# Kernel optimization log

Measured on AMD Instinct MI355X. Metric: run time of the kernel, lower is better.

## Reference

```python
import jax, jax.numpy as jnp
import numpy as np

B, C, H, W = 8, 256, 64, 64
C8 = C // 8


def setup_inputs() -> dict:
    key = jax.random.key(0)
    ks = jax.random.split(key, 8)
    x = jax.random.normal(ks[0], (B, C, H, W), dtype=jnp.float32)
    # 1x1 convs == channel matmuls; store as [out_ch, in_ch] plus bias
    Wq = jax.random.normal(ks[1], (C8, C), dtype=jnp.float32) * (1.0 / np.sqrt(C))
    bq = jnp.zeros((C8,), dtype=jnp.float32)
    Wk = jax.random.normal(ks[2], (C8, C), dtype=jnp.float32) * (1.0 / np.sqrt(C))
    bk = jnp.zeros((C8,), dtype=jnp.float32)
    Wv = jax.random.normal(ks[3], (C, C), dtype=jnp.float32) * (1.0 / np.sqrt(C))
    bv = jnp.zeros((C,), dtype=jnp.float32)
    # gamma initialized to zero in the module, but use a nonzero value so the
    # attention branch actually contributes to the output being checked
    gamma = jnp.full((1,), 0.5, dtype=jnp.float32)
    return {"x": x, "Wq": Wq, "bq": bq, "Wk": Wk, "bk": bk, "Wv": Wv, "bv": bv, "gamma": gamma}


def reference(x, Wq, bq, Wk, bk, Wv, bv, gamma):
    b, c, h, w = x.shape
    n = h * w
    xf = x.reshape(b, c, n)                                  # [B, C, N]
    q = jnp.einsum('oc,bcn->bon', Wq, xf) + bq[None, :, None]  # [B, C8, N]
    k = jnp.einsum('oc,bcn->bon', Wk, xf) + bk[None, :, None]  # [B, C8, N]
    v = jnp.einsum('oc,bcn->bon', Wv, xf) + bv[None, :, None]  # [B, C,  N]
    # attention[b, i, j] = sum_d q[b, d, i] * k[b, d, j]  (no 1/sqrt(d) scaling!)
    scores = jnp.einsum('bdi,bdj->bij', q, k)                # [B, N, N]
    attn = jax.nn.softmax(scores, axis=-1)                   # softmax over j
    # out[b, c, i] = sum_j v[b, c, j] * attn[b, i, j]
    out = jnp.einsum('bcj,bij->bci', v, attn)                # [B, C, N]
    out = out.reshape(b, c, h, w)
    return gamma[0] * out + x
```

## Files before the change

### kernel.cpp

```cpp
#include <hip/hip_runtime.h>
#include <math.h>

#define BB 8
#define CC 256
#define NN 4096

typedef float f4 __attribute__((ext_vector_type(4)));
typedef short bh8 __attribute__((ext_vector_type(8)));

__device__ __forceinline__ unsigned short f2bf(float f) {
    unsigned u = __builtin_bit_cast(unsigned, f);
    u += 0x7fff + ((u >> 16) & 1);
    return (unsigned short)(u >> 16);
}
__device__ __forceinline__ unsigned packbf(float a, float b) {
    return (unsigned)f2bf(a) | ((unsigned)f2bf(b) << 16);
}

__device__ __forceinline__ float exp2_fast(float x) {
    float r;
    asm("v_exp_f32 %0, %1" : "=v"(r) : "v"(x));
    return r;
}

__global__ void prep_w_kernel(const float* __restrict__ Wq, const float* __restrict__ bq,
                              const float* __restrict__ Wk, const float* __restrict__ bk,
                              const float* __restrict__ Wv, const float* __restrict__ bv,
                              float* __restrict__ WcatT, float* __restrict__ bcat) {
    const float L2E = 1.4426950408889634f;
    int idx = blockIdx.x * 256 + threadIdx.x;
    if (idx < 320) {
        bcat[idx] = (idx < 32) ? bq[idx] * L2E : (idx < 64 ? bk[idx - 32] : bv[idx - 64]);
    }
    if (idx < 320 * 256) {
        int o = idx >> 8;
        int c = idx & 255;
        float v = (o < 32) ? Wq[o * 256 + c] * L2E
                           : (o < 64 ? Wk[(o - 32) * 256 + c] : Wv[(o - 64) * 256 + c]);
        WcatT[c * 320 + o] = v;
    }
}

__global__ __launch_bounds__(256, 2) void qkv_kernel(
    const float* __restrict__ x, const float* __restrict__ WcatT,
    const float* __restrict__ bcat,
    unsigned short* __restrict__ q64, unsigned short* __restrict__ k64,
    unsigned short* __restrict__ vC) {
    __shared__ float xs[256 * 64];
    __shared__ unsigned short qkl[64 * 128];
    unsigned short* vsl = (unsigned short*)xs;

    int blk = blockIdx.x;
    int b = blk >> 6;
    int i0 = (blk & 63) << 6;
    int t = threadIdx.x;

    const float* xb = x + ((size_t)b << 20);
    for (int idx = t; idx < 256 * 64; idx += 256) {
        int c = idx >> 6, ii = idx & 63;
        xs[idx] = xb[((size_t)c << 12) + i0 + ii];
    }
    __syncthreads();

    int to = t & 63;
    int tp = t >> 6;

    float acc[80];
#pragma unroll
    for (int uo = 0; uo < 5; ++uo) {
        float bias = bcat[to + 64 * uo];
#pragma unroll
        for (int pi = 0; pi < 16; ++pi) acc[uo * 16 + pi] = bias;
    }

    for (int c = 0; c < 256; ++c) {
        const float* wc = WcatT + c * 320 + to;
        float w0 = wc[0];
        float w1 = wc[64];
        float w2 = wc[128];
        float w3 = wc[192];
        float w4 = wc[256];
        const float4* xr = (const float4*)(xs + c * 64 + 16 * tp);
#pragma unroll
        for (int q = 0; q < 4; ++q) {
            float4 xv = xr[q];
#pragma unroll
            for (int e = 0; e < 4; ++e) {
                int pi = 4 * q + e;
                float xe = (e == 0) ? xv.x : (e == 1) ? xv.y : (e == 2) ? xv.z : xv.w;
                acc[0 * 16 + pi] += w0 * xe;
                acc[1 * 16 + pi] += w1 * xe;
                acc[2 * 16 + pi] += w2 * xe;
                acc[3 * 16 + pi] += w3 * xe;
                acc[4 * 16 + pi] += w4 * xe;
            }
        }
    }
    __syncthreads();

#pragma unroll
    for (int pi = 0; pi < 16; ++pi) {
        int ii = 16 * tp + pi;
        float v = acc[pi];
        unsigned short hi = f2bf(v);
        float vhi = __builtin_bit_cast(float, ((unsigned)hi) << 16);
        unsigned short lo = f2bf(v - vhi);
        if (to < 32) {
            qkl[ii * 128 + to] = hi;
            qkl[ii * 128 + 32 + to] = lo;
        } else {
            qkl[ii * 128 + 32 + to] = hi;
            qkl[ii * 128 + 64 + to] = lo;
        }
    }
#pragma unroll
    for (int uo = 1; uo < 5; ++uo) {
#pragma unroll
        for (int pi = 0; pi < 16; ++pi) {
            int c = to + 64 * (uo - 1);
            int ii = 16 * tp + pi;
            vsl[c * 66 + ii] = f2bf(acc[uo * 16 + pi]);
        }
    }
    __syncthreads();

    const unsigned* qk32 = (const unsigned*)qkl;
    unsigned* qb = (unsigned*)(q64 + ((size_t)(b * NN + i0)) * 64);
    unsigned* kb = (unsigned*)(k64 + ((size_t)(b * NN + i0)) * 64);
    for (int idx = t; idx < 64 * 32; idx += 256) {
        int row = idx >> 5, dw = idx & 31;
        qb[row * 32 + dw] = qk32[row * 64 + dw];
        kb[row * 32 + dw] = qk32[row * 64 + 32 + dw];
    }
    for (int idx = t; idx < 256 * 32; idx += 256) {
        int c = idx >> 5, dw = idx & 31;
        unsigned val = *(const unsigned*)(vsl + c * 66 + 2 * dw);
        int i = 2 * dw;
        int p = 32 * (i >> 5) + 8 * ((i >> 2) & 3) + 4 * ((i >> 4) & 1) + (i & 3);
        *(unsigned*)(vC + ((size_t)(b * CC + c)) * NN + i0 + p) = val;
    }
}

__global__ __launch_bounds__(256, 2) void attn_kernel(
    const unsigned short* __restrict__ q64, const unsigned short* __restrict__ k64,
    const unsigned short* __restrict__ vC, const float* __restrict__ x,
    const float* __restrict__ gamma, float* __restrict__ out) {
    __shared__ unsigned short vs[2][256 * 64];

    int t = threadIdx.x;
    int lane = t & 63;
    int w = t >> 6;
    int g = lane >> 4;
    int li = lane & 15;
    int blk = blockIdx.x;
    int b = blk & 7;
    int i0 = (blk >> 3) << 6;
    int qb = i0 + 16 * w;

    const unsigned short* vb = vC + ((size_t)b * CC) * NN;
    const unsigned short* kb = k64 + ((size_t)b * NN) * 64;

    bh8 qf[2];
#pragma unroll
    for (int s = 0; s < 2; ++s)
        qf[s] = *(const bh8*)(q64 + ((size_t)(b * NN + qb + li)) * 64 + s * 32 + 8 * g);

    const unsigned short* vsrcb[8];
#pragma unroll
    for (int s = 0; s < 8; ++s) {
        int c = 64 * w + 8 * s + (lane >> 3);
        int slot = (lane & 7) ^ (c & 7);
        vsrcb[s] = vb + (size_t)c * NN + slot * 8;
    }
    const unsigned short* ksrcb[8];
#pragma unroll
    for (int jt = 0; jt < 4; ++jt)
#pragma unroll
        for (int s = 0; s < 2; ++s)
            ksrcb[jt * 2 + s] = kb + (size_t)(16 * jt + li) * 64 + s * 32 + 8 * g;

    f4 acc[16];
#pragma unroll
    for (int ct = 0; ct < 16; ++ct) acc[ct] = (f4){0.f, 0.f, 0.f, 0.f};
    float m = -INFINITY, l = 0.f;

    auto stageV = [&](int buf, int j0) {
#pragma unroll
        for (int s = 0; s < 8; ++s) {
            __builtin_amdgcn_global_load_lds(
                (const __attribute__((address_space(1))) unsigned int*)(vsrcb[s] + j0),
                (__attribute__((address_space(3))) unsigned int*)(&vs[buf][(64 * w + 8 * s) * 64]),
                16, 0, 0);
        }
    };
    auto loadK = [&](bh8 (&kf)[4][2], int j0) {
        size_t joff = (size_t)j0 * 64;
#pragma unroll
        for (int jt = 0; jt < 4; ++jt)
#pragma unroll
            for (int s = 0; s < 2; ++s)
                kf[jt][s] = *(const bh8*)(ksrcb[jt * 2 + s] + joff);
    };
    auto qkComp = [&](f4 (&sOut)[4], bh8 (&kc)[4][2]) {
#pragma unroll
        for (int jt = 0; jt < 4; ++jt) {
            f4 a = {0.f, 0.f, 0.f, 0.f};
            a = __builtin_amdgcn_mfma_f32_16x16x32_bf16(kc[jt][0], qf[0], a, 0, 0, 0);
            a = __builtin_amdgcn_mfma_f32_16x16x32_bf16(kc[jt][1], qf[0], a, 0, 0, 0);
            a = __builtin_amdgcn_mfma_f32_16x16x32_bf16(kc[jt][0], qf[1], a, 0, 0, 0);
            sOut[jt] = a;
        }
    };

    bh8 kf0[4][2], kf1[4][2];
    f4 sA[4], sB[4];

    stageV(0, 0);
    loadK(kf0, 0);
    loadK(kf1, 64);
    qkComp(sA, kf0);
    __syncthreads();

    auto step = [&](int tt, bh8 (&kNext)[4][2], bh8 (&kLoad)[4][2],
                    f4 (&sCur)[4], f4 (&sNxt)[4], int buf) {
        if (tt < 63) stageV(buf ^ 1, (tt + 1) << 6);
        if (tt < 62) loadK(kLoad, (tt + 2) << 6);

        if (tt < 63) qkComp(sNxt, kNext);

        float mx = sCur[0][0];
#pragma unroll
        for (int jt = 0; jt < 4; ++jt)
#pragma unroll
            for (int e = 0; e < 4; ++e) mx = fmaxf(mx, sCur[jt][e]);
        if (!__all(mx <= m + 11.541561f)) {
            mx = fmaxf(mx, __shfl_xor(mx, 16));
            mx = fmaxf(mx, __shfl_xor(mx, 32));
            float mnew = fmaxf(m, mx);
            float sc = exp2_fast(m - mnew);
            l *= sc;
#pragma unroll
            for (int ct = 0; ct < 16; ++ct)
#pragma unroll
                for (int e = 0; e < 4; ++e) acc[ct][e] *= sc;
            m = mnew;
        }
        float sum = 0.f;
#pragma unroll
        for (int jt = 0; jt < 4; ++jt)
#pragma unroll
            for (int e = 0; e < 4; ++e) {
                float p = exp2_fast(sCur[jt][e] - m);
                sCur[jt][e] = p;
                sum += p;
            }
        l += sum;

        const char* vsb = (const char*)vs[buf];
#pragma unroll
        for (int h = 0; h < 2; ++h) {
            union { unsigned u[4]; bh8 v; } pf;
            pf.u[0] = packbf(sCur[2 * h + 0][0], sCur[2 * h + 0][1]);
            pf.u[1] = packbf(sCur[2 * h + 0][2], sCur[2 * h + 0][3]);
            pf.u[2] = packbf(sCur[2 * h + 1][0], sCur[2 * h + 1][1]);
            pf.u[3] = packbf(sCur[2 * h + 1][2], sCur[2 * h + 1][3]);
            bh8 pb = pf.v;
            __builtin_amdgcn_s_setprio(1);
#pragma unroll
            for (int ct = 0; ct < 16; ++ct) {
                int c = 16 * ct + li;
                int off = c * 128 + ((64 * h + 16 * g) ^ ((c & 7) << 4));
                bh8 vf = *(const bh8*)(vsb + off);
                acc[ct] = __builtin_amdgcn_mfma_f32_16x16x32_bf16(vf, pb, acc[ct], 0, 0, 0);
            }
            __builtin_amdgcn_s_setprio(0);
        }
        __syncthreads();
    };

    for (int tt = 0; tt < 64; tt += 2) {
        step(tt, kf1, kf0, sA, sB, 0);
        step(tt + 1, kf0, kf1, sB, sA, 1);
    }

    l += __shfl_xor(l, 16);
    l += __shfl_xor(l, 32);

    float gm = gamma[0];
    float rl = 1.f / l;
    const float* xb = x + ((size_t)b * CC) * NN;
    float* ob = out + ((size_t)b * CC) * NN;
    int i = qb + li;
#pragma unroll
    for (int ct = 0; ct < 16; ++ct)
#pragma unroll
        for (int e = 0; e < 4; ++e) {
            int c = 16 * ct + 4 * g + e;
            size_t idx = (size_t)c * NN + i;
            ob[idx] = gm * (acc[ct][e] * rl) + xb[idx];
        }
}

extern "C" void kernel_launch(void* const* d_in, const int* in_sizes, int n_in,
                              void* d_out, int out_size, void* d_ws, size_t ws_size,
                              hipStream_t stream) {
    const float* x = (const float*)d_in[0];
    const float* Wq = (const float*)d_in[1];
    const float* bq = (const float*)d_in[2];
    const float* Wk = (const float*)d_in[3];
    const float* bk = (const float*)d_in[4];
    const float* Wv = (const float*)d_in[5];
    const float* bv = (const float*)d_in[6];
    const float* gamma = (const float*)d_in[7];
    float* out = (float*)d_out;

    unsigned short* ws16 = (unsigned short*)d_ws;
    unsigned short* q64w = ws16;
    unsigned short* k64w = ws16 + 2097152;
    unsigned short* vCw = ws16 + 4194304;
    float* WcatT = (float*)((char*)d_ws + 25165824);
    float* bcat = WcatT + 81920;

    prep_w_kernel<<<320, 256, 0, stream>>>(Wq, bq, Wk, bk, Wv, bv, WcatT, bcat);
    qkv_kernel<<<BB * (NN / 64), 256, 0, stream>>>(x, WcatT, bcat, q64w, k64w, vCw);
    attn_kernel<<<512, 256, 0, stream>>>(q64w, k64w, vCw, x, gamma, out);
}
```

Baseline: 235.9 us.

## Load V fragments directly from global memory instead of staging through LDS

Removes the double-buffered LDS staging of V tiles and the per-step __syncthreads, having each wave load its V MFMA operands straight from global memory into registers in interleaved batches. The launch bound is lowered to one block per SM to make room for the extra V registers. The aim is to drop barrier and LDS traffic, at the cost that the four waves in a block now each read the full V tile from global/L2, giving redundant loads and exposed latency, plus lower occupancy.

```diff
diff --git a/kernel.cpp b/kernel.cpp
--- a/kernel.cpp
+++ b/kernel.cpp
@@ -141,12 +141,10 @@
     }
 }
 
-__global__ __launch_bounds__(256, 2) void attn_kernel(
+__global__ __launch_bounds__(256, 1) void attn_kernel(
     const unsigned short* __restrict__ q64, const unsigned short* __restrict__ k64,
     const unsigned short* __restrict__ vC, const float* __restrict__ x,
     const float* __restrict__ gamma, float* __restrict__ out) {
-    __shared__ unsigned short vs[2][256 * 64];
-
     int t = threadIdx.x;
     int lane = t & 63;
     int w = t >> 6;
@@ -165,41 +163,24 @@
     for (int s = 0; s < 2; ++s)
         qf[s] = *(const bh8*)(q64 + ((size_t)(b * NN + qb + li)) * 64 + s * 32 + 8 * g);
 
-    const unsigned short* vsrcb[8];
-#pragma unroll
-    for (int s = 0; s < 8; ++s) {
-        int c = 64 * w + 8 * s + (lane >> 3);
-        int slot = (lane & 7) ^ (c & 7);
-        vsrcb[s] = vb + (size_t)c * NN + slot * 8;
-    }
-    const unsigned short* ksrcb[8];
-#pragma unroll
-    for (int jt = 0; jt < 4; ++jt)
-#pragma unroll
-        for (int s = 0; s < 2; ++s)
-            ksrcb[jt * 2 + s] = kb + (size_t)(16 * jt + li) * 64 + s * 32 + 8 * g;
+    const unsigned short* kbase = kb + (size_t)li * 64 + 8 * g;
+    const unsigned short* vbase = vb + (size_t)li * NN + 8 * g;
 
     f4 acc[16];
 #pragma unroll
     for (int ct = 0; ct < 16; ++ct) acc[ct] = (f4){0.f, 0.f, 0.f, 0.f};
     float m = -INFINITY, l = 0.f;
 
-    auto stageV = [&](int buf, int j0) {
-#pragma unroll
-        for (int s = 0; s < 8; ++s) {
-            __builtin_amdgcn_global_load_lds(
-                (const __attribute__((address_space(1))) unsigned int*)(vsrcb[s] + j0),
-                (__attribute__((address_space(3))) unsigned int*)(&vs[buf][(64 * w + 8 * s) * 64]),
-                16, 0, 0);
-        }
-    };
     auto loadK = [&](bh8 (&kf)[4][2], int j0) {
         size_t joff = (size_t)j0 * 64;
 #pragma unroll
         for (int jt = 0; jt < 4; ++jt)
 #pragma unroll
             for (int s = 0; s < 2; ++s)
-                kf[jt][s] = *(const bh8*)(ksrcb[jt * 2 + s] + joff);
+                kf[jt][s] = *(const bh8*)(kbase + joff + jt * (16 * 64) + s * 32);
+    };
+    auto vload = [&](int ct, int h, int j0) -> bh8 {
+        return *(const bh8*)(vbase + (size_t)ct * (16 * NN) + j0 + 32 * h);
     };
     auto qkComp = [&](f4 (&sOut)[4], bh8 (&kc)[4][2]) {
 #pragma unroll
@@ -215,18 +196,20 @@
     bh8 kf0[4][2], kf1[4][2];
     f4 sA[4], sB[4];
 
-    stageV(0, 0);
     loadK(kf0, 0);
     loadK(kf1, 64);
     qkComp(sA, kf0);
-    __syncthreads();
 
     auto step = [&](int tt, bh8 (&kNext)[4][2], bh8 (&kLoad)[4][2],
-                    f4 (&sCur)[4], f4 (&sNxt)[4], int buf) {
-        if (tt < 63) stageV(buf ^ 1, (tt + 1) << 6);
+                    f4 (&sCur)[4], f4 (&sNxt)[4]) {
+        int j0 = tt << 6;
         if (tt < 62) loadK(kLoad, (tt + 2) << 6);
 
         if (tt < 63) qkComp(sNxt, kNext);
+
+        bh8 va[8], vb2[8];
+#pragma unroll
+        for (int ct = 0; ct < 8; ++ct) va[ct] = vload(ct, 0, j0);
 
         float mx = sCur[0][0];
 #pragma unroll
@@ -256,31 +239,46 @@
             }
         l += sum;
 
-        const char* vsb = (const char*)vs[buf];
-#pragma unroll
-        for (int h = 0; h < 2; ++h) {
-            union { unsigned u[4]; bh8 v; } pf;
-            pf.u[0] = packbf(sCur[2 * h + 0][0], sCur[2 * h + 0][1]);
-            pf.u[1] = packbf(sCur[2 * h + 0][2], sCur[2 * h + 0][3]);
-            pf.u[2] = packbf(sCur[2 * h + 1][0], sCur[2 * h + 1][1]);
-            pf.u[3] = packbf(sCur[2 * h + 1][2], sCur[2 * h + 1][3]);
-            bh8 pb = pf.v;
-            __builtin_amdgcn_s_setprio(1);
-#pragma unroll
-            for (int ct = 0; ct < 16; ++ct) {
-                int c = 16 * ct + li;
-                int off = c * 128 + ((64 * h + 16 * g) ^ ((c & 7) << 4));
-                bh8 vf = *(const bh8*)(vsb + off);
-                acc[ct] = __builtin_amdgcn_mfma_f32_16x16x32_bf16(vf, pb, acc[ct], 0, 0, 0);
-            }
-            __builtin_amdgcn_s_setprio(0);
-        }
-        __syncthreads();
+        union { unsigned u[4]; bh8 v; } pf0, pf1;
+        pf0.u[0] = packbf(sCur[0][0], sCur[0][1]);
+        pf0.u[1] = packbf(sCur[0][2], sCur[0][3]);
+        pf0.u[2] = packbf(sCur[1][0], sCur[1][1]);
+        pf0.u[3] = packbf(sCur[1][2], sCur[1][3]);
+        pf1.u[0] = packbf(sCur[2][0], sCur[2][1]);
+        pf1.u[1] = packbf(sCur[2][2], sCur[2][3]);
+        pf1.u[2] = packbf(sCur[3][0], sCur[3][1]);
+        pf1.u[3] = packbf(sCur[3][2], sCur[3][3]);
+        bh8 pb0 = pf0.v, pb1 = pf1.v;
+
+#pragma unroll
+        for (int ct = 0; ct < 8; ++ct) vb2[ct] = vload(ct + 8, 0, j0);
+        __builtin_amdgcn_s_setprio(1);
+#pragma unroll
+        for (int ct = 0; ct < 8; ++ct)
+            acc[ct] = __builtin_amdgcn_mfma_f32_16x16x32_bf16(va[ct], pb0, acc[ct], 0, 0, 0);
+        __builtin_amdgcn_s_setprio(0);
+#pragma unroll
+        for (int ct = 0; ct < 8; ++ct) va[ct] = vload(ct, 1, j0);
+        __builtin_amdgcn_s_setprio(1);
+#pragma unroll
+        for (int ct = 0; ct < 8; ++ct)
+            acc[ct + 8] = __builtin_amdgcn_mfma_f32_16x16x32_bf16(vb2[ct], pb0, acc[ct + 8], 0, 0, 0);
+        __builtin_amdgcn_s_setprio(0);
+#pragma unroll
+        for (int ct = 0; ct < 8; ++ct) vb2[ct] = vload(ct + 8, 1, j0);
+        __builtin_amdgcn_s_setprio(1);
+#pragma unroll
+        for (int ct = 0; ct < 8; ++ct)
+            acc[ct] = __builtin_amdgcn_mfma_f32_16x16x32_bf16(va[ct], pb1, acc[ct], 0, 0, 0);
+#pragma unroll
+        for (int ct = 0; ct < 8; ++ct)
+            acc[ct + 8] = __builtin_amdgcn_mfma_f32_16x16x32_bf16(vb2[ct], pb1, acc[ct + 8], 0, 0, 0);
+        __builtin_amdgcn_s_setprio(0);
     };
 
     for (int tt = 0; tt < 64; tt += 2) {
-        step(tt, kf1, kf0, sA, sB, 0);
-        step(tt + 1, kf0, kf1, sB, sA, 1);
+        step(tt, kf1, kf0, sA, sB);
+        step(tt + 1, kf0, kf1, sB, sA);
     }
 
     l += __shfl_xor(l, 16);
```

Result: slower. 661.6 us (+180.5%).

## Compute QKV projection with split-bf16 MFMA instead of scalar FP32 FMAs

Applied to the files above, without the earlier changes.

The 1x1-conv QKV projection moves from scalar FP32 FMA loops to bf16 MFMA 16x16x32 instructions. Weights and inputs are split into hi/lo bf16 pairs to keep near-fp32 accuracy: three MFMAs per step for Q/K and two for V. Inputs are transposed into padded LDS, and the weight prep kernel now emits bf16 hi/lo arrays. This cuts the projection's ALU cost, but the extra split passes add MFMA work and V loses some precision.

```diff
diff --git a/kernel.cpp b/kernel.cpp
--- a/kernel.cpp
+++ b/kernel.cpp
@@ -26,7 +26,8 @@
 __global__ void prep_w_kernel(const float* __restrict__ Wq, const float* __restrict__ bq,
                               const float* __restrict__ Wk, const float* __restrict__ bk,
                               const float* __restrict__ Wv, const float* __restrict__ bv,
-                              float* __restrict__ WcatT, float* __restrict__ bcat) {
+                              unsigned short* __restrict__ Whi, unsigned short* __restrict__ Wlo,
+                              float* __restrict__ bcat) {
     const float L2E = 1.4426950408889634f;
     int idx = blockIdx.x * 256 + threadIdx.x;
     if (idx < 320) {
@@ -37,89 +38,118 @@
         int c = idx & 255;
         float v = (o < 32) ? Wq[o * 256 + c] * L2E
                            : (o < 64 ? Wk[(o - 32) * 256 + c] : Wv[(o - 64) * 256 + c]);
-        WcatT[c * 320 + o] = v;
+        unsigned short hi = f2bf(v);
+        float vhi = __builtin_bit_cast(float, ((unsigned)hi) << 16);
+        Whi[idx] = hi;
+        Wlo[idx] = f2bf(v - vhi);
     }
 }
 
 __global__ __launch_bounds__(256, 2) void qkv_kernel(
-    const float* __restrict__ x, const float* __restrict__ WcatT,
-    const float* __restrict__ bcat,
+    const float* __restrict__ x, const unsigned short* __restrict__ Whi,
+    const unsigned short* __restrict__ Wlo, const float* __restrict__ bcat,
     unsigned short* __restrict__ q64, unsigned short* __restrict__ k64,
     unsigned short* __restrict__ vC) {
-    __shared__ float xs[256 * 64];
-    __shared__ unsigned short qkl[64 * 128];
-    unsigned short* vsl = (unsigned short*)xs;
+    __shared__ __align__(16) char smem[67584];
+    unsigned short* xsTh = (unsigned short*)smem;
+    unsigned short* xsTl = (unsigned short*)(smem + 33792);
+    unsigned short* qkl = (unsigned short*)smem;
+    unsigned short* vsl = (unsigned short*)(smem + 16384);
 
     int blk = blockIdx.x;
     int b = blk >> 6;
     int i0 = (blk & 63) << 6;
     int t = threadIdx.x;
-
     const float* xb = x + ((size_t)b << 20);
+
     for (int idx = t; idx < 256 * 64; idx += 256) {
         int c = idx >> 6, ii = idx & 63;
-        xs[idx] = xb[((size_t)c << 12) + i0 + ii];
-    }
-    __syncthreads();
-
-    int to = t & 63;
-    int tp = t >> 6;
-
-    float acc[80];
-#pragma unroll
-    for (int uo = 0; uo < 5; ++uo) {
-        float bias = bcat[to + 64 * uo];
-#pragma unroll
-        for (int pi = 0; pi < 16; ++pi) acc[uo * 16 + pi] = bias;
-    }
-
-    for (int c = 0; c < 256; ++c) {
-        const float* wc = WcatT + c * 320 + to;
-        float w0 = wc[0];
-        float w1 = wc[64];
-        float w2 = wc[128];
-        float w3 = wc[192];
-        float w4 = wc[256];
-        const float4* xr = (const float4*)(xs + c * 64 + 16 * tp);
-#pragma unroll
-        for (int q = 0; q < 4; ++q) {
-            float4 xv = xr[q];
-#pragma unroll
-            for (int e = 0; e < 4; ++e) {
-                int pi = 4 * q + e;
-                float xe = (e == 0) ? xv.x : (e == 1) ? xv.y : (e == 2) ? xv.z : xv.w;
-                acc[0 * 16 + pi] += w0 * xe;
-                acc[1 * 16 + pi] += w1 * xe;
-                acc[2 * 16 + pi] += w2 * xe;
-                acc[3 * 16 + pi] += w3 * xe;
-                acc[4 * 16 + pi] += w4 * xe;
-            }
-        }
-    }
-    __syncthreads();
-
-#pragma unroll
-    for (int pi = 0; pi < 16; ++pi) {
-        int ii = 16 * tp + pi;
-        float v = acc[pi];
+        float v = xb[((size_t)c << 12) + i0 + ii];
         unsigned short hi = f2bf(v);
         float vhi = __builtin_bit_cast(float, ((unsigned)hi) << 16);
-        unsigned short lo = f2bf(v - vhi);
-        if (to < 32) {
-            qkl[ii * 128 + to] = hi;
-            qkl[ii * 128 + 32 + to] = lo;
-        } else {
-            qkl[ii * 128 + 32 + to] = hi;
-            qkl[ii * 128 + 64 + to] = lo;
-        }
-    }
-#pragma unroll
-    for (int uo = 1; uo < 5; ++uo) {
-#pragma unroll
-        for (int pi = 0; pi < 16; ++pi) {
-            int c = to + 64 * (uo - 1);
-            int ii = 16 * tp + pi;
-            vsl[c * 66 + ii] = f2bf(acc[uo * 16 + pi]);
+        xsTh[ii * 264 + c] = hi;
+        xsTl[ii * 264 + c] = f2bf(v - vhi);
+    }
+    __syncthreads();
+
+    int lane = t & 63;
+    int w = t >> 6;
+    int g = lane >> 4;
+    int li = lane & 15;
+
+    f4 acc[5][4];
+#pragma unroll
+    for (int tt = 0; tt < 5; ++tt)
+#pragma unroll
+        for (int it = 0; it < 4; ++it) acc[tt][it] = (f4){0.f, 0.f, 0.f, 0.f};
+
+#pragma unroll
+    for (int tt = 0; tt < 5; ++tt) {
+        int ot = w + 4 * tt;
+        bool qk = (ot < 4);
+        const unsigned short* wrh = Whi + (size_t)(16 * ot + li) * 256 + 8 * g;
+        const unsigned short* wrl = Wlo + (size_t)(16 * ot + li) * 256 + 8 * g;
+        bh8 ah[8], al[8];
+#pragma unroll
+        for (int ck = 0; ck < 8; ++ck) {
+            ah[ck] = *(const bh8*)(wrh + 32 * ck);
+            al[ck] = *(const bh8*)(wrl + 32 * ck);
+        }
+#pragma unroll
+        for (int it = 0; it < 4; ++it) {
+            const unsigned short* xrh = xsTh + (16 * it + li) * 264 + 8 * g;
+            const unsigned short* xrl = xsTl + (16 * it + li) * 264 + 8 * g;
+            f4 a = acc[tt][it];
+            if (qk) {
+#pragma unroll
+                for (int ck = 0; ck < 8; ++ck) {
+                    bh8 xh = *(const bh8*)(xrh + 32 * ck);
+                    bh8 xl = *(const bh8*)(xrl + 32 * ck);
+                    a = __builtin_amdgcn_mfma_f32_16x16x32_bf16(ah[ck], xh, a, 0, 0, 0);
+                    a = __builtin_amdgcn_mfma_f32_16x16x32_bf16(al[ck], xh, a, 0, 0, 0);
+                    a = __builtin_amdgcn_mfma_f32_16x16x32_bf16(ah[ck], xl, a, 0, 0, 0);
+                }
+            } else {
+#pragma unroll
+                for (int ck = 0; ck < 8; ++ck) {
+                    bh8 xh = *(const bh8*)(xrh + 32 * ck);
+                    a = __builtin_amdgcn_mfma_f32_16x16x32_bf16(ah[ck], xh, a, 0, 0, 0);
+                    a = __builtin_amdgcn_mfma_f32_16x16x32_bf16(al[ck], xh, a, 0, 0, 0);
+                }
+            }
+            acc[tt][it] = a;
+        }
+    }
+    __syncthreads();
+
+#pragma unroll
+    for (int tt = 0; tt < 5; ++tt) {
+        int ot = w + 4 * tt;
+        float bias[4];
+#pragma unroll
+        for (int e = 0; e < 4; ++e) bias[e] = bcat[16 * ot + 4 * g + e];
+#pragma unroll
+        for (int it = 0; it < 4; ++it) {
+            int ii = 16 * it + li;
+#pragma unroll
+            for (int e = 0; e < 4; ++e) {
+                int o = 16 * ot + 4 * g + e;
+                float v = acc[tt][it][e] + bias[e];
+                if (o < 64) {
+                    unsigned short hi = f2bf(v);
+                    float vhi = __builtin_bit_cast(float, ((unsigned)hi) << 16);
+                    unsigned short lo = f2bf(v - vhi);
+                    if (o < 32) {
+                        qkl[ii * 128 + o] = hi;
+                        qkl[ii * 128 + 32 + o] = lo;
+                    } else {
+                        qkl[ii * 128 + 32 + o] = hi;
+                        qkl[ii * 128 + 64 + o] = lo;
+                    }
+                } else {
+                    vsl[(o - 64) * 66 + ii] = f2bf(v);
+                }
+            }
         }
     }
     __syncthreads();
@@ -318,10 +348,11 @@
     unsigned short* q64w = ws16;
     unsigned short* k64w = ws16 + 2097152;
     unsigned short* vCw = ws16 + 4194304;
-    float* WcatT = (float*)((char*)d_ws + 25165824);
-    float* bcat = WcatT + 81920;
-
-    prep_w_kernel<<<320, 256, 0, stream>>>(Wq, bq, Wk, bk, Wv, bv, WcatT, bcat);
-    qkv_kernel<<<BB * (NN / 64), 256, 0, stream>>>(x, WcatT, bcat, q64w, k64w, vCw);
+    unsigned short* Whiw = ws16 + 12582912;
+    unsigned short* Wlow = Whiw + 81920;
+    float* bcatw = (float*)(Wlow + 81920);
+
+    prep_w_kernel<<<320, 256, 0, stream>>>(Wq, bq, Wk, bk, Wv, bv, Whiw, Wlow, bcatw);
+    qkv_kernel<<<BB * (NN / 64), 256, 0, stream>>>(x, Whiw, Wlow, bcatw, q64w, k64w, vCw);
     attn_kernel<<<512, 256, 0, stream>>>(q64w, k64w, vCw, x, gamma, out);
 }
```

New measurement: 205.5 us. 1.15x faster.
